# Kernel optimization log

Measured on AMD Instinct MI355X. Metric: run time of the kernel, lower is better.

Reference implementation:

```python
import jax, jax.numpy as jnp
import numpy as np
from jax.scipy.special import logsumexp

GROUP_LEN = 8
LABEL_SMOOTHING = 0.1
LOSS_TYPES = ("part_slice", "whole_slice", "part_block", "whole_block")
GN, D = 8192, 128


def setup_inputs() -> dict:
    key = jax.random.key(0)
    k1, k2 = jax.random.split(key)
    return {
        "image_features1": jax.random.normal(k1, (GN, D), dtype=jnp.float32),
        "image_features2": jax.random.normal(k2, (GN, D), dtype=jnp.float32),
        "logit_scale": jnp.float32(1.0 / 0.07),
    }


def _group_losses(S, G, N, eps):
    """Vectorized equivalents of the four Python-loop losses on an [GN,GN] logit matrix."""
    GN_ = G * N
    S4 = S.reshape(G, N, G, N)                      # [g, n, g2, n2]
    idx = jnp.arange(G)
    diag_blocks = S4[idx, :, idx, :]                # [G, N, N] (same-group blocks)

    # row-wise quantities
    row_lse = logsumexp(S, axis=1).reshape(G, N)    # [G, N]
    row_sum = S.sum(axis=1).reshape(G, N)           # [G, N]
    pos_sum = diag_blocks.sum(axis=-1)              # [G, N] sum over same-group cols

    # part_slice: mean_i (1-eps)(lse_i - pos_sum_i) + eps/(GN)(lse_i - row_sum_i)
    part_slice = jnp.mean((1.0 - eps) * (row_lse - pos_sum)
                          + (eps / GN_) * (row_lse - row_sum))

    # whole_slice: pos vector is row * y_i -> same-group entries plus (GN-N) zeros,
    # so lse(pos) = logaddexp(lse(diag entries), log(GN - N)) (exp(0)=1 per zero).
    diag_row_lse = logsumexp(diag_blocks, axis=-1)  # [G, N]
    pos_lse = jnp.logaddexp(diag_row_lse, jnp.log(jnp.float32(GN_ - N)))
    blk_row_lse = logsumexp(S4, axis=3)             # [G, N, G] per-row per-block lse
    ws_smooth = (row_lse[:, :, None] - blk_row_lse).sum(axis=-1)  # [G, N]
    whole_slice = jnp.mean((1.0 - eps) * (row_lse - pos_lse) + (eps / G) * ws_smooth)

    # group-level quantities
    grp_lse = logsumexp(S4, axis=(1, 2, 3))         # [G] lse over group's full row band
    grp_sum = S4.sum(axis=(1, 2, 3))                # [G]
    diag_sum = diag_blocks.sum(axis=(1, 2))         # [G]

    # part_block
    part_block = jnp.mean((1.0 - eps) * (grp_lse - diag_sum / (N * N))
                          + eps * (grp_lse - grp_sum / (G * N * N)))

    # whole_block
    blk_lse = logsumexp(S4, axis=(1, 3))            # [G, G] per block lse
    diag_blk_lse = blk_lse[idx, idx]                # [G]
    wb_smooth = (grp_lse[:, None] - blk_lse).sum(axis=-1)  # [G]
    whole_block = jnp.mean((1.0 - eps) * (grp_lse - diag_blk_lse) + (eps / G) * wb_smooth)

    return {"part_slice": part_slice, "whole_slice": whole_slice,
            "part_block": part_block, "whole_block": whole_block}


def reference(image_features1, image_features2, logit_scale):
    f1 = image_features1 / jnp.linalg.norm(image_features1, axis=-1, keepdims=True)
    f2 = image_features2 / jnp.linalg.norm(image_features2, axis=-1, keepdims=True)
    GN_, _ = f1.shape
    N = GROUP_LEN
    G = GN_ // N
    S1 = logit_scale * (f1 @ f2.T)                  # logits_per_image1 [GN, GN]
    S2 = S1.T                                       # logits_per_image2
    eps = LABEL_SMOOTHING
    l1 = _group_losses(S1, G, N, eps)
    l2 = _group_losses(S2, G, N, eps)
    loss = jnp.float32(0.0)
    for lt in LOSS_TYPES:
        loss = loss + 0.5 * (l1[lt] + l2[lt])
    return loss / len(LOSS_TYPES)
```

## Files before the change

### kernel.cpp

```cpp
#include <hip/hip_runtime.h>
#include <math.h>

typedef __attribute__((ext_vector_type(8))) short bf16x8;
typedef __attribute__((ext_vector_type(4))) float f32x4;
typedef unsigned short ushort_t;

#define GN 8192
#define NGRP 1024
#define DDIM 128
#define NCH 16
#define LOG2E 1.4426950408889634f
#define LN2 0.6931471805599453f

#if __has_builtin(__builtin_amdgcn_exp2f)
#define EXP2F(x) __builtin_amdgcn_exp2f(x)
#else
#define EXP2F(x) exp2f(x)
#endif
#if __has_builtin(__builtin_amdgcn_logf)
#define LOG2FAST(x) __builtin_amdgcn_logf(x)
#else
#define LOG2FAST(x) log2f(x)
#endif

#define ROWST 0
#define GRPB  (ROWST + GN*NCH*2)
#define DT    (GRPB + NGRP*NCH)
#define DU8   (DT + 2*GN)
#define GSUM  (DU8 + NGRP)
#define CSUMP (GSUM + 2*NGRP*DDIM)
#define COLP  (CSUMP + 2*32*DDIM)
#define GRP2P (COLP + 128*GN*2)
#define FIN2  (GRP2P + 128*NGRP)
#define SB2   (FIN2 + GN*2)
#define PART  (SB2 + NGRP)

__device__ __forceinline__ ushort_t f2bf(float x) {
  unsigned u = __float_as_uint(x);
  unsigned r = (u + 0x7fffu + ((u >> 16) & 1u)) >> 16;
  return (ushort_t)r;
}
__device__ __forceinline__ float bf2f(unsigned h) {
  return __uint_as_float(h << 16);
}

__device__ __forceinline__ float dpp_shr1_add(float v) {
  int s = __builtin_amdgcn_update_dpp(0, __float_as_int(v), 0x111, 0xF, 0xF, true);
  return v + __int_as_float(s);
}
__device__ __forceinline__ float dpp_shr2_add(float v) {
  int s = __builtin_amdgcn_update_dpp(0, __float_as_int(v), 0x112, 0xF, 0xF, true);
  return v + __int_as_float(s);
}
__device__ __forceinline__ float dpp_shr4_add(float v) {
  int s = __builtin_amdgcn_update_dpp(0, __float_as_int(v), 0x114, 0xF, 0xF, true);
  return v + __int_as_float(s);
}
__device__ __forceinline__ float dpp_ror8_add(float v) {
  int s = __builtin_amdgcn_update_dpp(0, __float_as_int(v), 0x128, 0xF, 0xF, true);
  return v + __int_as_float(s);
}

__global__ __launch_bounds__(256) void normg_kernel(
    const float* __restrict__ f1, const float* __restrict__ f2,
    const float* __restrict__ scp, ushort_t* __restrict__ wsu,
    float* __restrict__ wf) {
  const int b = blockIdx.x;
  const int m = b >> 10;
  const int g = b & 1023;
  const int t = threadIdx.x;
  const int r = t >> 5;
  const int c4 = t & 31;
  const float* __restrict__ f = m ? f2 : f1;
  const float fac0 = m ? 1.0f : (scp[0] * LOG2E);

  const float4 v = ((const float4*)(f + ((size_t)(g * 8 + r)) * DDIM))[c4];
  float ss = v.x * v.x + v.y * v.y + v.z * v.z + v.w * v.w;
  #pragma unroll
  for (int d = 1; d < 32; d <<= 1) ss += __shfl_xor(ss, d);
  const float inv = fac0 / sqrtf(ss);

  ushort4 o;
  o.x = f2bf(v.x * inv); o.y = f2bf(v.y * inv);
  o.z = f2bf(v.z * inv); o.w = f2bf(v.w * inv);
  ((ushort4*)(wsu + (size_t)m * GN * DDIM + (size_t)(g * 8 + r) * DDIM))[c4] = o;

  __shared__ float lds[8][DDIM];
  lds[r][c4 * 4 + 0] = bf2f(o.x);
  lds[r][c4 * 4 + 1] = bf2f(o.y);
  lds[r][c4 * 4 + 2] = bf2f(o.z);
  lds[r][c4 * 4 + 3] = bf2f(o.w);
  __syncthreads();
  if (t < DDIM) {
    float s = 0.f;
    #pragma unroll
    for (int j = 0; j < 8; ++j) s += lds[j][t];
    wf[GSUM + ((size_t)m * NGRP + g) * DDIM + t] = s;
  }
}

__global__ __launch_bounds__(128) void csum_kernel(float* __restrict__ wf) {
  const int b = blockIdx.x;
  const int m = b >> 5;
  const int seg = b & 31;
  const int k = threadIdx.x;
  const float* gp = wf + GSUM + ((size_t)m * NGRP + seg * 32) * DDIM + k;
  float s = 0.f;
  #pragma unroll 8
  for (int g = 0; g < 32; ++g) s += gp[(size_t)g * DDIM];
  wf[CSUMP + ((size_t)m * 32 + seg) * DDIM + k] = s;
}

__global__ __launch_bounds__(256, 4) void gemm_stats(
    const ushort_t* __restrict__ wsu, const float* __restrict__ scp,
    float* __restrict__ wf) {
  const int idx = blockIdx.x;
  const int rowblk = idx >> 4;
  const int chunk = idx & 15;
  const int t = threadIdx.x;
  const int w = t >> 6;
  const int l = t & 63;
  const int li = l & 15;
  const int q = l >> 4;
  const float C = scp[0];
  const float nC2 = -C * LOG2E;

  const ushort_t* A = wsu;
  const ushort_t* B = wsu + (size_t)GN * DDIM;
  const int row0 = rowblk * 64;

  __shared__ ushort_t As[64 * 128];
  {
    const int arow = t >> 2;
    const int aq = t & 3;
    const ushort_t* Agp = A + (size_t)(row0 + arow) * DDIM + aq * 32;
    #pragma unroll
    for (int j = 0; j < 4; ++j) {
      const int swz = (aq * 4 + j) ^ (arow & 15);
      *(uint4*)(As + arow * 128 + swz * 8) = *(const uint4*)(const void*)(Agp + j * 8);
    }
  }
  __syncthreads();

  float esum[4] = {0.f, 0.f, 0.f, 0.f};
  float sbl[4]  = {0.f, 0.f, 0.f, 0.f};
  float sBr[4]  = {0.f, 0.f, 0.f, 0.f};

  const ushort_t* Bp = B + ((size_t)(chunk * 512 + w * 16) + li) * DDIM + q * 8;
  const bool hasdia = (chunk == (row0 >> 9));
  const int idiag = (row0 & 511) >> 6;
  const f32x4 cinit = {nC2, nC2, nC2, nC2};

  #pragma unroll 1
  for (int i = 0; i < 8; ++i) {
    const ushort_t* Bi = Bp + (size_t)i * (64 * DDIM);
    bf16x8 bc[4];
    #pragma unroll
    for (int ks = 0; ks < 4; ++ks)
      bc[ks] = *(const bf16x8*)(const void*)(Bi + ks * 32);

    f32x4 acc[4];
    #pragma unroll
    for (int s = 0; s < 4; ++s) acc[s] = cinit;
    #pragma unroll
    for (int ks = 0; ks < 4; ++ks) {
      int co = (((ks * 4 + q) ^ li) * 8);
      asm volatile("" : "+v"(co));
      bf16x8 a0[4];
      #pragma unroll
      for (int s = 0; s < 4; ++s)
        a0[s] = *(const bf16x8*)(As + (16 * s + li) * 128 + co);
      #pragma unroll
      for (int s = 0; s < 4; ++s)
        acc[s] = __builtin_amdgcn_mfma_f32_16x16x32_bf16(bc[ks], a0[s], acc[s], 0, 0, 0);
    }

    const bool dia = hasdia && (i == idiag);
    const int cb = chunk * 512 + i * 64 + w * 16;
    float lvc = 0.f;
    float ecolp[4] = {0.f, 0.f, 0.f, 0.f};
    float prodc[4] = {1.f, 1.f, 1.f, 1.f};

    #pragma unroll
    for (int s = 0; s < 4; ++s) {
      float e[4];
      #pragma unroll
      for (int r = 0; r < 4; ++r) e[r] = EXP2F(acc[s][r]);
      float tt = (e[0] + e[1]) + (e[2] + e[3]);
      esum[s] += tt;
      float u = tt + __shfl_xor(tt, 16);
      sbl[s] += LOG2FAST(u);
      float bs = dpp_shr4_add(dpp_shr2_add(dpp_shr1_add(u)));
      float lg = LOG2FAST(bs);
      sBr[s] += lg;
      lvc += lg;

      #pragma unroll
      for (int r = 0; r < 4; ++r) {
        float o_ = dpp_shr4_add(dpp_shr2_add(dpp_shr1_add(e[r])));
        prodc[r] *= o_;
        ecolp[r] += o_;
        if (dia && w == s && ((li == 7 && q < 2) || (li == 15 && q >= 2)))
          wf[DT + GN + cb + q * 4 + r] = o_;
      }
      if (dia && w == s) {
        if (((q >> 1) == (li >> 3)) && ((q & 1) == 0))
          wf[DT + row0 + 16 * w + li] = u;
        if (l == 7)  wf[DU8 + rowblk * 8 + 2 * w]     = bs;
        if (l == 47) wf[DU8 + rowblk * 8 + 2 * w + 1] = bs;
      }
    }

    float lc[4];
    #pragma unroll
    for (int r = 0; r < 4; ++r) {
      ecolp[r] = dpp_ror8_add(ecolp[r]);
      lc[r] = LOG2FAST(prodc[r]);
      lc[r] = dpp_ror8_add(lc[r]);
    }
    lvc = dpp_ror8_add(lvc);
    if (li == 7) {
      #pragma unroll
      for (int r = 0; r < 4; ++r) {
        float2 st; st.x = ecolp[r]; st.y = lc[r];
        *(float2*)(wf + COLP + ((size_t)rowblk * GN + cb + q * 4 + r) * 2) = st;
      }
    }
    if (l == 7)  wf[GRP2P + (size_t)rowblk * NGRP + (cb >> 3)]     = lvc;
    if (l == 39) wf[GRP2P + (size_t)rowblk * NGRP + (cb >> 3) + 1] = lvc;
  }

  #pragma unroll
  for (int s = 0; s < 4; ++s) {
    esum[s] += __shfl_xor(esum[s], 16); esum[s] += __shfl_xor(esum[s], 32);
    sbl[s]  += __shfl_xor(sbl[s], 16);  sbl[s]  += __shfl_xor(sbl[s], 32);
    sBr[s]  += __shfl_xor(sBr[s], 16);  sBr[s]  += __shfl_xor(sBr[s], 32);
  }

  __shared__ float redE[4][64], redL[4][64], redB[4][8];
  if (q == 0) {
    #pragma unroll
    for (int s = 0; s < 4; ++s) {
      redE[w][16 * s + li] = esum[s];
      redL[w][16 * s + li] = 0.5f * sbl[s];
    }
  }
  if (l == 7) {
    #pragma unroll
    for (int s = 0; s < 4; ++s) redB[w][2 * s] = 0.5f * sBr[s];
  }
  if (l == 15) {
    #pragma unroll
    for (int s = 0; s < 4; ++s) redB[w][2 * s + 1] = 0.5f * sBr[s];
  }
  __syncthreads();

  if (t < 64) {
    const float E = redE[0][t] + redE[1][t] + redE[2][t] + redE[3][t];
    const float L = redL[0][t] + redL[1][t] + redL[2][t] + redL[3][t];
    const size_t o = ROWST + ((size_t)(row0 + t) * NCH + chunk) * 2;
    wf[o + 0] = E; wf[o + 1] = L;
  }
  if (t < 8) {
    const float s4 = redB[0][t] + redB[1][t] + redB[2][t] + redB[3][t];
    wf[GRPB + (size_t)(rowblk * 8 + t) * NCH + chunk] = s4;
  }
}

__global__ __launch_bounds__(256) void colred_kernel(float* __restrict__ wf) {
  const int b = blockIdx.x;
  const int t = threadIdx.x;
  const int lane = t & 31;
  const int slice = t >> 5;
  __shared__ float red[8][32][2];
  if (b < 256) {
    const int c = b * 32 + lane;
    float e = 0.f, ls = 0.f;
    #pragma unroll 4
    for (int k = 0; k < 16; ++k) {
      const int rb = slice * 16 + k;
      float2 v = *(const float2*)(wf + COLP + ((size_t)rb * GN + c) * 2);
      e += v.x; ls += v.y;
    }
    red[slice][lane][0] = e; red[slice][lane][1] = ls;
    __syncthreads();
    if (slice == 0) {
      float E = 0.f, L = 0.f;
      #pragma unroll
      for (int s2 = 0; s2 < 8; ++s2) { E += red[s2][lane][0]; L += red[s2][lane][1]; }
      wf[FIN2 + c * 2] = E; wf[FIN2 + c * 2 + 1] = L;
    }
  } else {
    const int cg = (b - 256) * 32 + lane;
    float s = 0.f;
    #pragma unroll 4
    for (int k = 0; k < 16; ++k) s += wf[GRP2P + (size_t)(slice * 16 + k) * NGRP + cg];
    red[slice][lane][0] = s;
    __syncthreads();
    if (slice == 0) {
      float S = 0.f;
      #pragma unroll
      for (int s2 = 0; s2 < 8; ++s2) S += red[s2][lane][0];
      wf[SB2 + cg] = S;
    }
  }
}

__global__ __launch_bounds__(256) void loss_kernel(
    const float* __restrict__ wf, const ushort_t* __restrict__ wsu,
    const float* __restrict__ scp, float* __restrict__ partials) {
  const int b = blockIdx.x;
  const int pass = b >> 5;
  const int rbase = (b & 31) * 256;
  const int t = threadIdx.x;
  const int row = rbase + t;
  const int g = row >> 3;
  const float C = scp[0];
  const float eps = 0.1f;

  __shared__ float cs_l[DDIM];
  if (t < DDIM) {
    const float* cp = wf + CSUMP + ((size_t)(pass ^ 1) * 32) * DDIM + t;
    float s = 0.f;
    #pragma unroll 8
    for (int seg = 0; seg < 32; ++seg) s += cp[(size_t)seg * DDIM];
    cs_l[t] = s;
  }
  __syncthreads();

  float E, L;
  if (pass == 0) {
    const size_t ro = ROWST + ((size_t)row * NCH) * 2;
    E = 0.f; L = 0.f;
    #pragma unroll
    for (int ch = 0; ch < NCH; ++ch) {
      E += wf[ro + 2 * ch];
      L += wf[ro + 2 * ch + 1];
    }
  } else {
    E = wf[FIN2 + row * 2];
    L = wf[FIN2 + row * 2 + 1];
  }

  const ushort_t* M = wsu + (size_t)pass * GN * DDIM + (size_t)row * DDIM;
  const float* gs = wf + GSUM + ((size_t)(pass ^ 1) * NGRP + g) * DDIM;
  float r2 = 0.f, p2 = 0.f;
  const uint4* Mv = (const uint4*)(const void*)M;
  #pragma unroll
  for (int c = 0; c < 8; ++c) {
    uint4 vv = Mv[c];
    unsigned uu[4] = {vv.x, vv.y, vv.z, vv.w};
    #pragma unroll
    for (int j = 0; j < 4; ++j) {
      float flo = bf2f(uu[j] & 0xffffu);
      float fhi = bf2f(uu[j] >> 16);
      const int k = c * 8 + j * 2;
      r2 += flo * cs_l[k];   r2 += fhi * cs_l[k + 1];
      p2 += flo * gs[k];     p2 += fhi * gs[k + 1];
    }
  }
  const float R = LN2 * r2;
  const float P = LN2 * p2;

  const float Td = wf[DT + (size_t)pass * GN + row];
  const float logE = __logf(E);
  const float row_lse = C + logE;

  float acc = ((1.f - eps) * (row_lse - P) + (eps / 8192.f) * (row_lse - R)) * (1.f / 8192.f);
  const float dl = C + __logf(Td);
  const float l8 = 9.0099363f;
  const float mx = fmaxf(dl, l8);
  const float pos_lse = mx + __logf(__expf(dl - mx) + __expf(l8 - mx));
  acc += ((1.f - eps) * (row_lse - pos_lse) + (eps / 1024.f) * (1024.f * logE - LN2 * L)) * (1.f / 8192.f);

  __shared__ float shE[256], shR[256], shP[256];
  shE[t] = E; shR[t] = R; shP[t] = P;
  __syncthreads();
  if (t < 32) {
    float Eg = 0.f, Rg = 0.f, Pg = 0.f;
    #pragma unroll
    for (int j = 0; j < 8; ++j) { Eg += shE[t * 8 + j]; Rg += shR[t * 8 + j]; Pg += shP[t * 8 + j]; }
    const int g2 = (rbase >> 3) + t;
    float SB;
    if (pass == 0) {
      SB = 0.f;
      #pragma unroll
      for (int ch = 0; ch < NCH; ++ch) SB += wf[GRPB + (size_t)g2 * NCH + ch];
    } else {
      SB = wf[SB2 + g2];
    }
    const float U = wf[DU8 + g2];
    const float logEg = __logf(Eg);
    const float grp_lse = C + logEg;
    acc += ((1.f - eps) * (grp_lse - Pg * (1.f / 64.f)) + eps * (grp_lse - Rg * (1.f / 65536.f))) * (1.f / 1024.f);
    const float dbl = C + __logf(U);
    acc += ((1.f - eps) * (grp_lse - dbl) + (eps / 1024.f) * (1024.f * logEg - LN2 * SB)) * (1.f / 1024.f);
  }

  #pragma unroll
  for (int d = 1; d < 64; d <<= 1) acc += __shfl_xor(acc, d);
  __shared__ float sr[4];
  if ((t & 63) == 0) sr[t >> 6] = acc;
  __syncthreads();
  if (t == 0) partials[b] = sr[0] + sr[1] + sr[2] + sr[3];
}

__global__ __launch_bounds__(64) void final_kernel(
    const float* __restrict__ partials, float* __restrict__ out) {
  const int t = threadIdx.x;
  float v = partials[t];
  #pragma unroll
  for (int d = 1; d < 64; d <<= 1) v += __shfl_xor(v, d);
  if (t == 0) out[0] = 0.125f * v;
}

extern "C" void kernel_launch(void* const* d_in, const int* in_sizes, int n_in,
                              void* d_out, int out_size, void* d_ws, size_t ws_size,
                              hipStream_t stream) {
  const float* f1 = (const float*)d_in[0];
  const float* f2 = (const float*)d_in[1];
  const float* sc = (const float*)d_in[2];
  ushort_t* wsu = (ushort_t*)d_ws;
  float* wf = (float*)((char*)d_ws + (size_t)2 * GN * DDIM * sizeof(ushort_t));
  float* out = (float*)d_out;

  hipLaunchKernelGGL(normg_kernel, dim3(2048), dim3(256), 0, stream, f1, f2, sc, wsu, wf);
  hipLaunchKernelGGL(csum_kernel, dim3(64), dim3(128), 0, stream, wf);
  hipLaunchKernelGGL(gemm_stats, dim3(2048), dim3(256), 0, stream, wsu, sc, wf);
  hipLaunchKernelGGL(colred_kernel, dim3(288), dim3(256), 0, stream, wf);
  hipLaunchKernelGGL(loss_kernel, dim3(64), dim3(256), 0, stream, wf, wsu, sc, wf + PART);
  hipLaunchKernelGGL(final_kernel, dim3(1), dim3(64), 0, stream, wf + PART, out);
}
```

Measured before the change: 68.14 us.

## Compute transposed tile via second MFMA to replace DPP column reductions

```diff
diff --git a/kernel.cpp b/kernel.cpp
--- a/kernel.cpp
+++ b/kernel.cpp
@@ -159,9 +159,9 @@
     for (int ks = 0; ks < 4; ++ks)
       bc[ks] = *(const bf16x8*)(const void*)(Bi + ks * 32);
 
-    f32x4 acc[4];
-    #pragma unroll
-    for (int s = 0; s < 4; ++s) acc[s] = cinit;
+    f32x4 accs[4], accn[4];
+    #pragma unroll
+    for (int s = 0; s < 4; ++s) { accs[s] = cinit; accn[s] = cinit; }
     #pragma unroll
     for (int ks = 0; ks < 4; ++ks) {
       int co = (((ks * 4 + q) ^ li) * 8);
@@ -171,22 +171,25 @@
       for (int s = 0; s < 4; ++s)
         a0[s] = *(const bf16x8*)(As + (16 * s + li) * 128 + co);
       #pragma unroll
-      for (int s = 0; s < 4; ++s)
-        acc[s] = __builtin_amdgcn_mfma_f32_16x16x32_bf16(bc[ks], a0[s], acc[s], 0, 0, 0);
+      for (int s = 0; s < 4; ++s) {
+        accs[s] = __builtin_amdgcn_mfma_f32_16x16x32_bf16(bc[ks], a0[s], accs[s], 0, 0, 0);
+        accn[s] = __builtin_amdgcn_mfma_f32_16x16x32_bf16(a0[s], bc[ks], accn[s], 0, 0, 0);
+      }
     }
 
     const bool dia = hasdia && (i == idiag);
     const int cb = chunk * 512 + i * 64 + w * 16;
     float lvc = 0.f;
-    float ecolp[4] = {0.f, 0.f, 0.f, 0.f};
-    float prodc[4] = {1.f, 1.f, 1.f, 1.f};
+    float ecol = 0.f;
+    float prodo = 1.f;
 
     #pragma unroll
     for (int s = 0; s < 4; ++s) {
-      float e[4];
-      #pragma unroll
-      for (int r = 0; r < 4; ++r) e[r] = EXP2F(acc[s][r]);
-      float tt = (e[0] + e[1]) + (e[2] + e[3]);
+      float e0 = EXP2F(accs[s][0]);
+      float e1 = EXP2F(accs[s][1]);
+      float e2_ = EXP2F(accs[s][2]);
+      float e3 = EXP2F(accs[s][3]);
+      float tt = (e0 + e1) + (e2_ + e3);
       esum[s] += tt;
       float u = tt + __shfl_xor(tt, 16);
       sbl[s] += LOG2FAST(u);
@@ -194,38 +197,37 @@
       float lg = LOG2FAST(bs);
       sBr[s] += lg;
       lvc += lg;
-
-      #pragma unroll
-      for (int r = 0; r < 4; ++r) {
-        float o_ = dpp_shr4_add(dpp_shr2_add(dpp_shr1_add(e[r])));
-        prodc[r] *= o_;
-        ecolp[r] += o_;
-        if (dia && w == s && ((li == 7 && q < 2) || (li == 15 && q >= 2)))
-          wf[DT + GN + cb + q * 4 + r] = o_;
-      }
       if (dia && w == s) {
         if (((q >> 1) == (li >> 3)) && ((q & 1) == 0))
           wf[DT + row0 + 16 * w + li] = u;
         if (l == 7)  wf[DU8 + rowblk * 8 + 2 * w]     = bs;
         if (l == 47) wf[DU8 + rowblk * 8 + 2 * w + 1] = bs;
       }
-    }
-
-    float lc[4];
-    #pragma unroll
-    for (int r = 0; r < 4; ++r) {
-      ecolp[r] = dpp_ror8_add(ecolp[r]);
-      lc[r] = LOG2FAST(prodc[r]);
-      lc[r] = dpp_ror8_add(lc[r]);
-    }
+
+      float f0 = EXP2F(accn[s][0]);
+      float f1v = EXP2F(accn[s][1]);
+      float f2v = EXP2F(accn[s][2]);
+      float f3 = EXP2F(accn[s][3]);
+      float tt2 = (f0 + f1v) + (f2v + f3);
+      ecol += tt2;
+      float oct = tt2 + __shfl_xor(tt2, 16);
+      prodo *= oct * 16777216.0f;
+      if (dia && s == w && ((q >> 1) == (li >> 3)) && ((q & 1) == 0))
+        wf[DT + GN + cb + li] = oct;
+    }
+
+    ecol += __shfl_xor(ecol, 16);
+    ecol += __shfl_xor(ecol, 32);
+    float lgo = LOG2FAST(prodo) - 96.0f;
+    lgo += __shfl_xor(lgo, 16);
+    lgo += __shfl_xor(lgo, 32);
+    lgo *= 0.5f;
+    if (q == 0) {
+      float2 st; st.x = ecol; st.y = lgo;
+      *(float2*)(wf + COLP + ((size_t)rowblk * GN + cb + li) * 2) = st;
+    }
+
     lvc = dpp_ror8_add(lvc);
-    if (li == 7) {
-      #pragma unroll
-      for (int r = 0; r < 4; ++r) {
-        float2 st; st.x = ecolp[r]; st.y = lc[r];
-        *(float2*)(wf + COLP + ((size_t)rowblk * GN + cb + q * 4 + r) * 2) = st;
-      }
-    }
     if (l == 7)  wf[GRP2P + (size_t)rowblk * NGRP + (cb >> 3)]     = lvc;
     if (l == 39) wf[GRP2P + (size_t)rowblk * NGRP + (cb >> 3) + 1] = lvc;
   }
```

Measured after the change: 70.30 us. 3.2% more time.

## Replace partial-stat buffers and column reduction kernel with global atomic accumulation

Applied to the files above, without the earlier changes.

```diff
diff --git a/kernel.cpp b/kernel.cpp
--- a/kernel.cpp
+++ b/kernel.cpp
@@ -8,7 +8,6 @@
 #define GN 8192
 #define NGRP 1024
 #define DDIM 128
-#define NCH 16
 #define LOG2E 1.4426950408889634f
 #define LN2 0.6931471805599453f
 
@@ -23,17 +22,16 @@
 #define LOG2FAST(x) log2f(x)
 #endif
 
-#define ROWST 0
-#define GRPB  (ROWST + GN*NCH*2)
-#define DT    (GRPB + NGRP*NCH)
+#define ROW0  0
+#define SB0   (ROW0 + GN*2)
+#define FIN2  (SB0 + NGRP)
+#define SB2   (FIN2 + GN*2)
+#define ZEND  (SB2 + NGRP)
+#define DT    ZEND
 #define DU8   (DT + 2*GN)
 #define GSUM  (DU8 + NGRP)
 #define CSUMP (GSUM + 2*NGRP*DDIM)
-#define COLP  (CSUMP + 2*32*DDIM)
-#define GRP2P (COLP + 128*GN*2)
-#define FIN2  (GRP2P + 128*NGRP)
-#define SB2   (FIN2 + GN*2)
-#define PART  (SB2 + NGRP)
+#define PART  (CSUMP + 2*32*DDIM)
 
 __device__ __forceinline__ ushort_t f2bf(float x) {
   unsigned u = __float_as_uint(x);
@@ -69,6 +67,8 @@
   const int m = b >> 10;
   const int g = b & 1023;
   const int t = threadIdx.x;
+  if (t < 17) wf[b * 17 + t] = 0.f;
+
   const int r = t >> 5;
   const int c4 = t & 31;
   const float* __restrict__ f = m ? f2 : f1;
@@ -222,12 +222,12 @@
     if (li == 7) {
       #pragma unroll
       for (int r = 0; r < 4; ++r) {
-        float2 st; st.x = ecolp[r]; st.y = lc[r];
-        *(float2*)(wf + COLP + ((size_t)rowblk * GN + cb + q * 4 + r) * 2) = st;
+        atomicAdd(&wf[FIN2 + (size_t)(cb + q * 4 + r) * 2],     ecolp[r]);
+        atomicAdd(&wf[FIN2 + (size_t)(cb + q * 4 + r) * 2 + 1], lc[r]);
       }
     }
-    if (l == 7)  wf[GRP2P + (size_t)rowblk * NGRP + (cb >> 3)]     = lvc;
-    if (l == 39) wf[GRP2P + (size_t)rowblk * NGRP + (cb >> 3) + 1] = lvc;
+    if (l == 7)  atomicAdd(&wf[SB2 + (cb >> 3)],     lvc);
+    if (l == 39) atomicAdd(&wf[SB2 + (cb >> 3) + 1], lvc);
   }
 
   #pragma unroll
@@ -258,51 +258,12 @@
   if (t < 64) {
     const float E = redE[0][t] + redE[1][t] + redE[2][t] + redE[3][t];
     const float L = redL[0][t] + redL[1][t] + redL[2][t] + redL[3][t];
-    const size_t o = ROWST + ((size_t)(row0 + t) * NCH + chunk) * 2;
-    wf[o + 0] = E; wf[o + 1] = L;
+    atomicAdd(&wf[ROW0 + (size_t)(row0 + t) * 2],     E);
+    atomicAdd(&wf[ROW0 + (size_t)(row0 + t) * 2 + 1], L);
   }
   if (t < 8) {
     const float s4 = redB[0][t] + redB[1][t] + redB[2][t] + redB[3][t];
-    wf[GRPB + (size_t)(rowblk * 8 + t) * NCH + chunk] = s4;
-  }
-}
-
-__global__ __launch_bounds__(256) void colred_kernel(float* __restrict__ wf) {
-  const int b = blockIdx.x;
-  const int t = threadIdx.x;
-  const int lane = t & 31;
-  const int slice = t >> 5;
-  __shared__ float red[8][32][2];
-  if (b < 256) {
-    const int c = b * 32 + lane;
-    float e = 0.f, ls = 0.f;
-    #pragma unroll 4
-    for (int k = 0; k < 16; ++k) {
-      const int rb = slice * 16 + k;
-      float2 v = *(const float2*)(wf + COLP + ((size_t)rb * GN + c) * 2);
-      e += v.x; ls += v.y;
-    }
-    red[slice][lane][0] = e; red[slice][lane][1] = ls;
-    __syncthreads();
-    if (slice == 0) {
-      float E = 0.f, L = 0.f;
-      #pragma unroll
-      for (int s2 = 0; s2 < 8; ++s2) { E += red[s2][lane][0]; L += red[s2][lane][1]; }
-      wf[FIN2 + c * 2] = E; wf[FIN2 + c * 2 + 1] = L;
-    }
-  } else {
-    const int cg = (b - 256) * 32 + lane;
-    float s = 0.f;
-    #pragma unroll 4
-    for (int k = 0; k < 16; ++k) s += wf[GRP2P + (size_t)(slice * 16 + k) * NGRP + cg];
-    red[slice][lane][0] = s;
-    __syncthreads();
-    if (slice == 0) {
-      float S = 0.f;
-      #pragma unroll
-      for (int s2 = 0; s2 < 8; ++s2) S += red[s2][lane][0];
-      wf[SB2 + cg] = S;
-    }
+    atomicAdd(&wf[SB0 + rowblk * 8 + t], s4);
   }
 }
 
@@ -328,19 +289,9 @@
   }
   __syncthreads();
 
-  float E, L;
-  if (pass == 0) {
-    const size_t ro = ROWST + ((size_t)row * NCH) * 2;
-    E = 0.f; L = 0.f;
-    #pragma unroll
-    for (int ch = 0; ch < NCH; ++ch) {
-      E += wf[ro + 2 * ch];
-      L += wf[ro + 2 * ch + 1];
-    }
-  } else {
-    E = wf[FIN2 + row * 2];
-    L = wf[FIN2 + row * 2 + 1];
-  }
+  const size_t eo = (pass == 0 ? ROW0 : FIN2) + (size_t)row * 2;
+  const float E = wf[eo];
+  const float L = wf[eo + 1];
 
   const ushort_t* M = wsu + (size_t)pass * GN * DDIM + (size_t)row * DDIM;
   const float* gs = wf + GSUM + ((size_t)(pass ^ 1) * NGRP + g) * DDIM;
@@ -381,14 +332,7 @@
     #pragma unroll
     for (int j = 0; j < 8; ++j) { Eg += shE[t * 8 + j]; Rg += shR[t * 8 + j]; Pg += shP[t * 8 + j]; }
     const int g2 = (rbase >> 3) + t;
-    float SB;
-    if (pass == 0) {
-      SB = 0.f;
-      #pragma unroll
-      for (int ch = 0; ch < NCH; ++ch) SB += wf[GRPB + (size_t)g2 * NCH + ch];
-    } else {
-      SB = wf[SB2 + g2];
-    }
+    const float SB = wf[(pass == 0 ? SB0 : SB2) + g2];
     const float U = wf[DU8 + g2];
     const float logEg = __logf(Eg);
     const float grp_lse = C + logEg;
@@ -427,7 +371,6 @@
   hipLaunchKernelGGL(normg_kernel, dim3(2048), dim3(256), 0, stream, f1, f2, sc, wsu, wf);
   hipLaunchKernelGGL(csum_kernel, dim3(64), dim3(128), 0, stream, wf);
   hipLaunchKernelGGL(gemm_stats, dim3(2048), dim3(256), 0, stream, wsu, sc, wf);
-  hipLaunchKernelGGL(colred_kernel, dim3(288), dim3(256), 0, stream, wf);
   hipLaunchKernelGGL(loss_kernel, dim3(64), dim3(256), 0, stream, wf, wsu, sc, wf + PART);
   hipLaunchKernelGGL(final_kernel, dim3(1), dim3(64), 0, stream, wf + PART, out);
 }
```

Measured after the change: 149.2 us. 119% more time.

## Batch log2 calls via scaled products and fold csum into colred

Applied to the files above, without the earlier changes.

```diff
diff --git a/kernel.cpp b/kernel.cpp
--- a/kernel.cpp
+++ b/kernel.cpp
@@ -97,18 +97,6 @@
     for (int j = 0; j < 8; ++j) s += lds[j][t];
     wf[GSUM + ((size_t)m * NGRP + g) * DDIM + t] = s;
   }
-}
-
-__global__ __launch_bounds__(128) void csum_kernel(float* __restrict__ wf) {
-  const int b = blockIdx.x;
-  const int m = b >> 5;
-  const int seg = b & 31;
-  const int k = threadIdx.x;
-  const float* gp = wf + GSUM + ((size_t)m * NGRP + seg * 32) * DDIM + k;
-  float s = 0.f;
-  #pragma unroll 8
-  for (int g = 0; g < 32; ++g) s += gp[(size_t)g * DDIM];
-  wf[CSUMP + ((size_t)m * 32 + seg) * DDIM + k] = s;
 }
 
 __global__ __launch_bounds__(256, 4) void gemm_stats(
@@ -145,6 +133,8 @@
   float esum[4] = {0.f, 0.f, 0.f, 0.f};
   float sbl[4]  = {0.f, 0.f, 0.f, 0.f};
   float sBr[4]  = {0.f, 0.f, 0.f, 0.f};
+  float pu[4]   = {1.f, 1.f, 1.f, 1.f};
+  float pbs[4]  = {1.f, 1.f, 1.f, 1.f};
 
   const ushort_t* Bp = B + ((size_t)(chunk * 512 + w * 16) + li) * DDIM + q * 8;
   const bool hasdia = (chunk == (row0 >> 9));
@@ -177,7 +167,7 @@
 
     const bool dia = hasdia && (i == idiag);
     const int cb = chunk * 512 + i * 64 + w * 16;
-    float lvc = 0.f;
+    float lvcP = 1.f;
     float ecolp[4] = {0.f, 0.f, 0.f, 0.f};
     float prodc[4] = {1.f, 1.f, 1.f, 1.f};
 
@@ -189,20 +179,22 @@
       float tt = (e[0] + e[1]) + (e[2] + e[3]);
       esum[s] += tt;
       float u = tt + __shfl_xor(tt, 16);
-      sbl[s] += LOG2FAST(u);
-      float bs = dpp_shr4_add(dpp_shr2_add(dpp_shr1_add(u)));
-      float lg = LOG2FAST(bs);
-      sBr[s] += lg;
-      lvc += lg;
-
+      pu[s] *= u * 262144.f;
+
+      float o_[4];
       #pragma unroll
       for (int r = 0; r < 4; ++r) {
-        float o_ = dpp_shr4_add(dpp_shr2_add(dpp_shr1_add(e[r])));
-        prodc[r] *= o_;
-        ecolp[r] += o_;
+        o_[r] = dpp_shr4_add(dpp_shr2_add(dpp_shr1_add(e[r])));
+        prodc[r] *= o_[r] * 16777216.f;
+        ecolp[r] += o_[r];
         if (dia && w == s && ((li == 7 && q < 2) || (li == 15 && q >= 2)))
-          wf[DT + GN + cb + q * 4 + r] = o_;
+          wf[DT + GN + cb + q * 4 + r] = o_[r];
       }
+      float sr_ = (o_[0] + o_[1]) + (o_[2] + o_[3]);
+      float bs = sr_ + __shfl_xor(sr_, 16);
+      lvcP *= bs * 65536.f;
+      pbs[s] *= bs * 16384.f;
+
       if (dia && w == s) {
         if (((q >> 1) == (li >> 3)) && ((q & 1) == 0))
           wf[DT + row0 + 16 * w + li] = u;
@@ -211,13 +203,24 @@
       }
     }
 
+    if ((i & 3) == 3) {
+      #pragma unroll
+      for (int s = 0; s < 4; ++s) {
+        sbl[s] += LOG2FAST(pu[s]) - 72.f;
+        pu[s] = 1.f;
+        sBr[s] += LOG2FAST(pbs[s]) - 56.f;
+        pbs[s] = 1.f;
+      }
+    }
+
     float lc[4];
     #pragma unroll
     for (int r = 0; r < 4; ++r) {
       ecolp[r] = dpp_ror8_add(ecolp[r]);
-      lc[r] = LOG2FAST(prodc[r]);
+      lc[r] = LOG2FAST(prodc[r]) - 96.f;
       lc[r] = dpp_ror8_add(lc[r]);
     }
+    float lvc = LOG2FAST(lvcP) - 64.f;
     lvc = dpp_ror8_add(lvc);
     if (li == 7) {
       #pragma unroll
@@ -290,7 +293,7 @@
       for (int s2 = 0; s2 < 8; ++s2) { E += red[s2][lane][0]; L += red[s2][lane][1]; }
       wf[FIN2 + c * 2] = E; wf[FIN2 + c * 2 + 1] = L;
     }
-  } else {
+  } else if (b < 288) {
     const int cg = (b - 256) * 32 + lane;
     float s = 0.f;
     #pragma unroll 4
@@ -302,6 +305,17 @@
       #pragma unroll
       for (int s2 = 0; s2 < 8; ++s2) S += red[s2][lane][0];
       wf[SB2 + cg] = S;
+    }
+  } else {
+    const int b2 = b - 288;
+    const int m = b2 >> 5;
+    const int seg = b2 & 31;
+    if (t < DDIM) {
+      const float* gp = wf + GSUM + ((size_t)m * NGRP + seg * 32) * DDIM + t;
+      float s = 0.f;
+      #pragma unroll 8
+      for (int g = 0; g < 32; ++g) s += gp[(size_t)g * DDIM];
+      wf[CSUMP + ((size_t)m * 32 + seg) * DDIM + t] = s;
     }
   }
 }
@@ -425,9 +439,8 @@
   float* out = (float*)d_out;
 
   hipLaunchKernelGGL(normg_kernel, dim3(2048), dim3(256), 0, stream, f1, f2, sc, wsu, wf);
-  hipLaunchKernelGGL(csum_kernel, dim3(64), dim3(128), 0, stream, wf);
   hipLaunchKernelGGL(gemm_stats, dim3(2048), dim3(256), 0, stream, wsu, sc, wf);
-  hipLaunchKernelGGL(colred_kernel, dim3(288), dim3(256), 0, stream, wf);
+  hipLaunchKernelGGL(colred_kernel, dim3(352), dim3(256), 0, stream, wf);
   hipLaunchKernelGGL(loss_kernel, dim3(64), dim3(256), 0, stream, wf, wsu, sc, wf + PART);
   hipLaunchKernelGGL(final_kernel, dim3(1), dim3(64), 0, stream, wf + PART, out);
 }
```

After: 66.95 us. About the same (-1.7%).
